# Kernel tuning notes

Measured on AMD Instinct MI355X. Metric: run time of the kernel, lower is better.

The kernel has to match this reference:

```python
import jax, jax.numpy as jnp
import numpy as np

B, DIM, H, W = 8, 128, 128, 128
QK, MLP, HEADS, NT, GS = 128, 256, 4, 8, 128


def _ln(x, w, b):
    m = jnp.mean(x, -1, keepdims=True)
    v = jnp.mean((x - m) ** 2, -1, keepdims=True)
    return (x - m) * jax.lax.rsqrt(v + 1e-5) * w + b


def _norml2(x):
    n = jnp.sqrt(jnp.sum(x * x, -1, keepdims=True))
    return x / jnp.maximum(n, 1e-12)


def setup_inputs() -> dict:
    key = jax.random.key(0)
    ks = jax.random.split(key, 12)
    s = 0.02
    f32 = jnp.float32
    return {
        'x': jax.random.normal(ks[0], (B, DIM, H, W), f32),
        'means': jax.random.normal(ks[1], (NT, DIM), f32),
        'ln1_w': jnp.ones((DIM,), f32), 'ln1_b': jnp.zeros((DIM,), f32),
        'wq': jax.random.normal(ks[2], (QK, DIM), f32) * s,
        'wk': jax.random.normal(ks[3], (QK, DIM), f32) * s,
        'wv': jax.random.normal(ks[4], (DIM, DIM), f32) * s,
        'wproj': jax.random.normal(ks[5], (DIM, DIM), f32) * s,
        'irca_wk': jax.random.normal(ks[6], (QK, DIM), f32) * s,
        'irca_wv': jax.random.normal(ks[7], (DIM, DIM), f32) * s,
        'conv1x1_w': jax.random.normal(ks[8], (DIM, DIM), f32) * s,
        'ln2_w': jnp.ones((DIM,), f32), 'ln2_b': jnp.zeros((DIM,), f32),
        'fc1_w': jax.random.normal(ks[9], (MLP, DIM), f32) * s,
        'fc1_b': jnp.zeros((MLP,), f32),
        'dw_w': jax.random.normal(ks[10], (MLP, 1, 5, 5), f32) * s,
        'dw_b': jnp.zeros((MLP,), f32),
        'fc2_w': jax.random.normal(ks[11], (DIM, MLP), f32) * s,
        'fc2_b': jnp.zeros((DIM,), f32),
    }


def reference(x, means, ln1_w, ln1_b, wq, wk, wv, wproj, irca_wk, irca_wv,
              conv1x1_w, ln2_w, ln2_b, fc1_w, fc1_b, dw_w, dw_b, fc2_w, fc2_b):
    Bx, C, Hh, Ww = x.shape
    N = Hh * Ww
    xt = x.reshape(Bx, C, N).transpose(0, 2, 1)          # b n c
    residual = xt
    xn = _ln(xt, ln1_w, ln1_b)
    m = jax.lax.stop_gradient(means)                      # eval: means buffer, detached
    # IRCA (eval path): global K/V from cluster means
    dq, dv = QK // HEADS, C // HEADS
    kg = (m @ irca_wk.T).reshape(NT, HEADS, dq).transpose(1, 0, 2)  # h nt dq
    vg = (m @ irca_wv.T).reshape(NT, HEADS, dv).transpose(1, 0, 2)  # h nt dv
    # cluster assignment -> token reordering (no grad)
    scores = jnp.einsum('bic,jc->bij', _norml2(xn), _norml2(m))
    buckets = jnp.argmax(scores, axis=-1)
    idx = jnp.argsort(buckets, axis=-1)                   # [B,N] permutation
    # IASA
    q = xn @ wq.T
    k = xn @ wk.T
    v = xn @ wv.T
    take = lambda t: jnp.take_along_axis(t, idx[:, :, None], axis=1)
    q, k, v = take(q), take(k), take(v)
    gs = min(N, GS)
    ng = (N + gs - 1) // gs
    pad_n = ng * gs - N
    qp = jnp.concatenate([q, jnp.flip(q[:, N - pad_n:N], axis=1)], axis=1)
    qp = qp.reshape(Bx, ng, gs, HEADS, dq).transpose(0, 1, 3, 2, 4)  # b g h gs dq

    def window(t, d):
        tp = jnp.concatenate([t, jnp.flip(t[:, N - pad_n - gs:N], axis=1)], axis=1)
        blk = tp.reshape(Bx, ng + 1, gs, HEADS, d)
        win = jnp.concatenate([blk[:, :-1], blk[:, 1:]], axis=2)     # b g 2gs h d
        return win.transpose(0, 1, 3, 2, 4)

    kp = window(k, dq)
    vp = window(v, dv)
    scale = 1.0 / np.sqrt(dq)
    a1 = jax.nn.softmax(jnp.einsum('bghqd,bghkd->bghqk', qp, kp) * scale, axis=-1)
    out1 = jnp.einsum('bghqk,bghkd->bghqd', a1, vp)
    a2 = jax.nn.softmax(jnp.einsum('bghqd,hkd->bghqk', qp, kg) * scale, axis=-1)
    out2 = jnp.einsum('bghqk,hkd->bghqd', a2, vg)
    out = (out1 + out2).transpose(0, 1, 3, 2, 4).reshape(Bx, ng * gs, C)[:, :N]
    inv = jnp.argsort(idx, axis=-1)                       # scatter-back = inverse perm
    out = jnp.take_along_axis(out, inv[:, :, None], axis=1)
    out = out @ wproj.T
    yimg = out.transpose(0, 2, 1).reshape(Bx, C, Hh, Ww)
    yimg = jnp.einsum('oc,bchw->bohw', conv1x1_w, yimg)
    x2 = residual + yimg.reshape(Bx, C, N).transpose(0, 2, 1)
    # ConvFFN with PreNorm
    xm = _ln(x2, ln2_w, ln2_b)
    h1 = jax.nn.gelu(xm @ fc1_w.T + fc1_b, approximate=False)
    himg = h1.transpose(0, 2, 1).reshape(Bx, MLP, Hh, Ww)
    dwc = jax.lax.conv_general_dilated(himg, dw_w, (1, 1), 'SAME',
                                       feature_group_count=MLP,
                                       dimension_numbers=('NCHW', 'OIHW', 'NCHW'))
    dwc = jax.nn.gelu(dwc + dw_b.reshape(1, MLP, 1, 1), approximate=False)
    h1 = h1 + dwc.reshape(Bx, MLP, N).transpose(0, 2, 1)
    x3 = x2 + (h1 @ fc2_w.T + fc2_b)
    return x3.transpose(0, 2, 1).reshape(Bx, C, Hh, Ww)
```

## Files before the change

kernel.cpp:

```cpp
#include <hip/hip_runtime.h>
#include <math.h>

typedef unsigned short u16;
typedef unsigned int u32;
typedef __attribute__((ext_vector_type(8))) short bf16x8;
typedef __attribute__((ext_vector_type(4))) float f32x4;

constexpr int BB   = 8;
constexpr int DIMC = 128;
constexpr int HH   = 128;
constexpr int WW   = 128;
constexpr int NTOK = HH * WW;
constexpr int QKD  = 128;
constexpr int MLPD = 256;
constexpr int NTm  = 8;
constexpr int GSZ  = 128;
constexpr int NGRP = NTOK / GSZ;
constexpr size_t BIG = 16777216;

__device__ __forceinline__ float gelu_f(float v) {
    return 0.5f * v * (1.0f + erff(v * 0.70710678118654752440f));
}
__device__ __forceinline__ float b2f(u16 u) {
    return __uint_as_float(((u32)u) << 16);
}
__device__ __forceinline__ u16 f2b(float f) {
    u32 x = __float_as_uint(f);
    return (u16)((x + 0x7fffu + ((x >> 16) & 1u)) >> 16);
}
__device__ __forceinline__ float ulo(u32 u) { return __uint_as_float(u << 16); }
__device__ __forceinline__ float uhi(u32 u) { return __uint_as_float(u & 0xffff0000u); }

__global__ __launch_bounds__(128) void k_prep(const float* __restrict__ means,
        const float* __restrict__ iwk, const float* __restrict__ iwv,
        float* __restrict__ mhat, u16* __restrict__ kgbb, u16* __restrict__ vgtb) {
    __shared__ float sm[DIMC];
    __shared__ float inv_s;
    int tt = blockIdx.x;
    int t = threadIdx.x;
    sm[t] = means[tt * DIMC + t];
    __syncthreads();
    if (t == 0) {
        float s = 0.f;
        for (int c = 0; c < DIMC; c++) s += sm[c] * sm[c];
        inv_s = 1.f / fmaxf(sqrtf(s), 1e-12f);
    }
    __syncthreads();
    mhat[tt * DIMC + t] = sm[t] * inv_s;
    float sk = 0.f, sv = 0.f;
    #pragma unroll 8
    for (int c = 0; c < DIMC; c++) {
        sk = fmaf(sm[c], iwk[t * DIMC + c], sk);
        sv = fmaf(sm[c], iwv[t * DIMC + c], sv);
    }
    kgbb[tt * DIMC + t] = f2b(sk);
    vgtb[(t >> 5) * 256 + (t & 31) * 8 + tt] = f2b(sv);
}

__global__ __launch_bounds__(256) void k_cvtall(const float* __restrict__ wq,
        const float* __restrict__ wk, const float* __restrict__ wv,
        const float* __restrict__ fc1, const float* __restrict__ fc2,
        u16* __restrict__ wqkv, u16* __restrict__ fc1b, u16* __restrict__ fc2b) {
    int i = blockIdx.x * 256 + threadIdx.x;
    if (i < 49152) {
        const float* s = (i < 16384) ? wq : (i < 32768 ? wk : wv);
        wqkv[i] = f2b(s[i & 16383]);
    } else if (i < 81920) {
        fc1b[i - 49152] = f2b(fc1[i - 49152]);
    } else if (i < 114688) {
        fc2b[i - 81920] = f2b(fc2[i - 81920]);
    }
}

__global__ __launch_bounds__(256) void k_fuse(const float* __restrict__ c1,
        const float* __restrict__ wp, u16* __restrict__ wf) {
    __shared__ float wpS[DIMC * DIMC];
    int t = threadIdx.x;
    for (int i = t; i < DIMC * DIMC; i += 256) wpS[i] = wp[i];
    __syncthreads();
    int o = blockIdx.x * 2 + (t >> 7);
    int c = t & 127;
    float s = 0.f;
    #pragma unroll 8
    for (int m = 0; m < DIMC; m++) s = fmaf(c1[o * DIMC + m], wpS[m * DIMC + c], s);
    wf[o * DIMC + c] = f2b(s);
}

__global__ __launch_bounds__(256) void k_ln1(const float* __restrict__ x,
        const float* __restrict__ lw, const float* __restrict__ lb,
        const float* __restrict__ mhat, u16* __restrict__ xn, int* __restrict__ bucket) {
    __shared__ float smh[NTm * DIMC];
    __shared__ float lwb[DIMC], lbb[DIMC];
    __shared__ float red[4][64][3];
    __shared__ float scr[4][64][9];
    const int chunk = blockIdx.x;
    const int b = chunk >> 8;
    const int n0 = (chunk & 255) << 6;
    const int t = threadIdx.x;
    const int cg = t >> 6, tok = t & 63;
    const int n = n0 + tok;
    const int cbase = cg * 32;
    for (int i = t; i < NTm * DIMC; i += 256) smh[i] = mhat[i];
    if (t < DIMC) { lwb[t] = lw[t]; lbb[t] = lb[t]; }

    const float* xb = x + (size_t)b * DIMC * NTOK + (size_t)cbase * NTOK + n;
    float xv[32];
    float sum = 0.f, sq = 0.f;
    #pragma unroll
    for (int c = 0; c < 32; c++) {
        float v = xb[(size_t)c * NTOK];
        xv[c] = v;
        sum += v; sq += v * v;
    }
    red[cg][tok][0] = sum;
    red[cg][tok][1] = sq;
    __syncthreads();
    float s0 = red[0][tok][0] + red[1][tok][0] + red[2][tok][0] + red[3][tok][0];
    float q0 = red[0][tok][1] + red[1][tok][1] + red[2][tok][1] + red[3][tok][1];
    float mean = s0 * (1.0f / DIMC);
    float var = q0 * (1.0f / DIMC) - mean * mean;
    float rstd = rsqrtf(var + 1e-5f);

    float sc[NTm];
    #pragma unroll
    for (int j = 0; j < NTm; j++) sc[j] = 0.f;
    u32 opk[16];
    #pragma unroll
    for (int c = 0; c < 32; c += 2) {
        float v0 = (xv[c]     - mean) * rstd * lwb[cbase + c]     + lbb[cbase + c];
        float v1 = (xv[c + 1] - mean) * rstd * lwb[cbase + c + 1] + lbb[cbase + c + 1];
        #pragma unroll
        for (int j = 0; j < NTm; j++) {
            sc[j] = fmaf(v0, smh[j * DIMC + cbase + c], sc[j]);
            sc[j] = fmaf(v1, smh[j * DIMC + cbase + c + 1], sc[j]);
        }
        opk[c >> 1] = (u32)f2b(v0) | ((u32)f2b(v1) << 16);
    }
    u16* xnr = xn + ((size_t)b * NTOK + n) * DIMC + cbase;
    *(uint4*)(xnr + 0)  = make_uint4(opk[0],  opk[1],  opk[2],  opk[3]);
    *(uint4*)(xnr + 8)  = make_uint4(opk[4],  opk[5],  opk[6],  opk[7]);
    *(uint4*)(xnr + 16) = make_uint4(opk[8],  opk[9],  opk[10], opk[11]);
    *(uint4*)(xnr + 24) = make_uint4(opk[12], opk[13], opk[14], opk[15]);

    #pragma unroll
    for (int j = 0; j < NTm; j++) scr[cg][tok][j] = sc[j];
    __syncthreads();
    if (cg == 0) {
        int best = 0; float bv = 0.f;
        #pragma unroll
        for (int j = 0; j < NTm; j++) {
            float v = ((scr[0][tok][j] + scr[1][tok][j]) +
                       (scr[2][tok][j] + scr[3][tok][j]));
            if (j == 0 || v > bv) { bv = v; best = (v > bv || j == 0) ? ((j == 0) ? 0 : j) : best; }
        }
        float v0 = ((scr[0][tok][0] + scr[1][tok][0]) + (scr[2][tok][0] + scr[3][tok][0]));
        best = 0; bv = v0;
        #pragma unroll
        for (int j = 1; j < NTm; j++) {
            float v = ((scr[0][tok][j] + scr[1][tok][j]) + (scr[2][tok][j] + scr[3][tok][j]));
            if (v > bv) { bv = v; best = j; }
        }
        bucket[b * NTOK + n] = best;
    }
}

__global__ __launch_bounds__(64) void k_count(const int* __restrict__ bucket, int* __restrict__ cnt) {
    int chunk = blockIdx.x;
    int bk = bucket[(chunk << 6) + threadIdx.x];
    #pragma unroll
    for (int j = 0; j < NTm; j++) {
        unsigned long long m = __ballot(bk == j);
        if (threadIdx.x == 0) cnt[chunk * NTm + j] = (int)__popcll(m);
    }
}

__global__ __launch_bounds__(64) void k_scan(const int* __restrict__ cnt, int* __restrict__ base) {
    __shared__ int sc[256 * NTm];
    __shared__ int bb[NTm], tot[NTm];
    int b = blockIdx.x, t = threadIdx.x;
    for (int i = t; i < 256 * NTm; i += 64) sc[i] = cnt[b * 256 * NTm + i];
    __syncthreads();
    if (t < NTm) {
        int run = 0;
        for (int c = 0; c < 256; c++) {
            int v = sc[c * NTm + t];
            sc[c * NTm + t] = run;
            run += v;
        }
        tot[t] = run;
    }
    __syncthreads();
    if (t == 0) {
        int a = 0;
        for (int j = 0; j < NTm; j++) { bb[j] = a; a += tot[j]; }
    }
    __syncthreads();
    for (int i = t; i < 256 * NTm; i += 64) base[b * 256 * NTm + i] = sc[i] + bb[i & 7];
}

__global__ __launch_bounds__(64) void k_place(const int* __restrict__ bucket,
        const int* __restrict__ base, int* __restrict__ gidx) {
    int chunk = blockIdx.x;
    int lane = threadIdx.x;
    int nf = (chunk << 6) + lane;
    int bk = bucket[nf];
    unsigned long long lower = (1ull << lane) - 1ull;
    int rank = 0;
    #pragma unroll
    for (int j = 0; j < NTm; j++) {
        unsigned long long m = __ballot(bk == j);
        if (bk == j) rank = (int)__popcll(m & lower);
    }
    int b = nf >> 14;
    int pos = base[chunk * NTm + bk] + rank;
    gidx[b * NTOK + pos] = nf & (NTOK - 1);
}

__global__ __launch_bounds__(256) void k_inv(const int* __restrict__ gidx, u16* __restrict__ iinv) {
    int i = blockIdx.x * 256 + threadIdx.x;
    int b = i >> 14;
    iinv[((size_t)b << 14) + gidx[i]] = (u16)(i & (NTOK - 1));
}

template<int KDIM, int NOUT, int GATHER, int AIMG, int BIASF, int GELUF, int RES, int STIMG, int CBF, int LN2F>
__global__ __launch_bounds__(256) void g_mfma(const u16* __restrict__ A, const u16* __restrict__ W,
        const float* __restrict__ bias, const void* __restrict__ resid,
        const int* __restrict__ gidx, void* __restrict__ Cout, float ascale,
        const float* __restrict__ lnw, const float* __restrict__ lnb, void* __restrict__ Cout2) {
    __shared__ u16 As[128 * 40];
    __shared__ u16 Ws[128 * 40];
    const int b = blockIdx.z;
    const int m0 = blockIdx.x * 128;
    const int n0 = blockIdx.y * 128;
    const int t = threadIdx.x;
    const int lane = t & 63;
    const int wave = t >> 6;
    const int wm = (wave & 1) * 64;
    const int wn = (wave >> 1) * 64;
    const int srow = t >> 2;
    const int sko = (t & 3) * 8;
    const u16* pA0 = nullptr; const u16* pA1 = nullptr;
    if (!AIMG) {
        int ra0 = m0 + srow, ra1 = m0 + 64 + srow;
        if (GATHER == 1) {
            ra0 = gidx[b * NTOK + ra0];
            ra1 = gidx[b * NTOK + ra1];
        } else if (GATHER == 2) {
            const u16* gi = (const u16*)gidx;
            ra0 = gi[b * NTOK + ra0];
            ra1 = gi[b * NTOK + ra1];
        }
        pA0 = A + ((size_t)b * NTOK + ra0) * KDIM + sko;
        pA1 = A + ((size_t)b * NTOK + ra1) * KDIM + sko;
    }
    const u16* pW0 = W + (size_t)(n0 + srow) * KDIM + sko;
    const u16* pW1 = W + (size_t)(n0 + 64 + srow) * KDIM + sko;

    f32x4 acc[4][4];
    #pragma unroll
    for (int i = 0; i < 4; i++)
        #pragma unroll
        for (int j = 0; j < 4; j++) acc[i][j] = (f32x4){0.f, 0.f, 0.f, 0.f};

    for (int k0 = 0; k0 < KDIM; k0 += 32) {
        uint4 a0, a1, w0, w1;
        u16 e[16];
        if (!AIMG) {
            a0 = *(const uint4*)(pA0 + k0);
            a1 = *(const uint4*)(pA1 + k0);
        } else {
            const int kk2 = t & 31;
            const int tg = t >> 5;
            const u16* src = A + ((size_t)b * KDIM + k0 + kk2) * NTOK + m0 + tg * 16;
            *(uint4*)&e[0] = *(const uint4*)src;
            *(uint4*)&e[8] = *(const uint4*)(src + 8);
        }
        w0 = *(const uint4*)(pW0 + k0);
        w1 = *(const uint4*)(pW1 + k0);
        __syncthreads();
        if (!AIMG) {
            *(uint4*)&As[srow * 40 + sko] = a0;
            *(uint4*)&As[(64 + srow) * 40 + sko] = a1;
        } else {
            const int kk2 = t & 31;
            const int tg = t >> 5;
            #pragma unroll
            for (int j = 0; j < 16; j++) As[(tg * 16 + j) * 40 + kk2] = e[j];
        }
        *(uint4*)&Ws[srow * 40 + sko] = w0;
        *(uint4*)&Ws[(64 + srow) * 40 + sko] = w1;
        __syncthreads();
        bf16x8 af[4], bfv[4];
        #pragma unroll
        for (int i = 0; i < 4; i++)
            af[i] = *(bf16x8*)&As[(wm + i * 16 + (lane & 15)) * 40 + (lane >> 4) * 8];
        #pragma unroll
        for (int j = 0; j < 4; j++)
            bfv[j] = *(bf16x8*)&Ws[(wn + j * 16 + (lane & 15)) * 40 + (lane >> 4) * 8];
        #pragma unroll
        for (int i = 0; i < 4; i++)
            #pragma unroll
            for (int j = 0; j < 4; j++)
                acc[i][j] = __builtin_amdgcn_mfma_f32_16x16x32_bf16(af[i], bfv[j], acc[i][j], 0, 0, 0);
    }

    const int c2 = lane & 15, gq2 = lane >> 4;
    int colj[4];
    #pragma unroll
    for (int j = 0; j < 4; j++) colj[j] = n0 + wn + j * 16 + c2;

    if (LN2F) {
        #pragma unroll
        for (int i = 0; i < 4; i++) {
            int rbase = m0 + wm + i * 16 + gq2 * 4;
            #pragma unroll
            for (int j = 0; j < 4; j++) {
                const float* rf = (const float*)resid;
                float4 rr = *(const float4*)&rf[((size_t)b * NOUT + colj[j]) * NTOK + rbase];
                acc[i][j][0] += rr.x; acc[i][j][1] += rr.y;
                acc[i][j][2] += rr.z; acc[i][j][3] += rr.w;
            }
        }
        __syncthreads();
        float* ps = (float*)&As[0];
        const int h = wn >> 6;
        float mean_[4][4], rstd_[4][4];
        #pragma unroll
        for (int i = 0; i < 4; i++)
            #pragma unroll
            for (int r = 0; r < 4; r++) {
                float s = 0.f, q = 0.f;
                #pragma unroll
                for (int j = 0; j < 4; j++) { float tv = acc[i][j][r]; s += tv; q += tv * tv; }
                s += __shfl_xor(s, 1, 64); q += __shfl_xor(q, 1, 64);
                s += __shfl_xor(s, 2, 64); q += __shfl_xor(q, 2, 64);
                s += __shfl_xor(s, 4, 64); q += __shfl_xor(q, 4, 64);
                s += __shfl_xor(s, 8, 64); q += __shfl_xor(q, 8, 64);
                if (c2 == 0) {
                    int rl = wm + i * 16 + gq2 * 4 + r;
                    ps[(h * 128 + rl) * 2 + 0] = s;
                    ps[(h * 128 + rl) * 2 + 1] = q;
                }
            }
        __syncthreads();
        #pragma unroll
        for (int i = 0; i < 4; i++)
            #pragma unroll
            for (int r = 0; r < 4; r++) {
                int rl = wm + i * 16 + gq2 * 4 + r;
                float s = ps[rl * 2 + 0] + ps[(128 + rl) * 2 + 0];
                float q = ps[rl * 2 + 1] + ps[(128 + rl) * 2 + 1];
                float mn = s * (1.0f / 128.0f);
                float vr = q * (1.0f / 128.0f) - mn * mn;
                mean_[i][r] = mn;
                rstd_[i][r] = rsqrtf(vr + 1e-5f);
            }
        float lwj[4], lbj[4];
        #pragma unroll
        for (int j = 0; j < 4; j++) { lwj[j] = lnw[colj[j]]; lbj[j] = lnb[colj[j]]; }
        u16* xo = (u16*)Cout;
        u16* mo = (u16*)Cout2;
        #pragma unroll
        for (int i = 0; i < 4; i++) {
            int rbase = m0 + wm + i * 16 + gq2 * 4;
            #pragma unroll
            for (int j = 0; j < 4; j++)
                #pragma unroll
                for (int r = 0; r < 4; r++) {
                    float tv = acc[i][j][r];
                    size_t off = ((size_t)b * NTOK + rbase + r) * NOUT + colj[j];
                    xo[off] = f2b(tv);
                    mo[off] = f2b((tv - mean_[i][r]) * rstd_[i][r] * lwj[j] + lbj[j]);
                }
        }
        return;
    }

    const float smul = (blockIdx.y == 0) ? ascale : 1.0f;
    float bj[4];
    #pragma unroll
    for (int j = 0; j < 4; j++) bj[j] = BIASF ? bias[colj[j]] : 0.f;
    #pragma unroll
    for (int i = 0; i < 4; i++) {
        int rbase = m0 + wm + i * 16 + gq2 * 4;
        #pragma unroll
        for (int j = 0; j < 4; j++) {
            f32x4 v = acc[i][j];
            v[0] *= smul; v[1] *= smul; v[2] *= smul; v[3] *= smul;
            if (BIASF) { v[0] += bj[j]; v[1] += bj[j]; v[2] += bj[j]; v[3] += bj[j]; }
            if (GELUF) { v[0] = gelu_f(v[0]); v[1] = gelu_f(v[1]); v[2] = gelu_f(v[2]); v[3] = gelu_f(v[3]); }
            if (RES == 1) {
                const float* rf = (const float*)resid;
                float4 rr = *(const float4*)&rf[((size_t)b * NOUT + colj[j]) * NTOK + rbase];
                v[0] += rr.x; v[1] += rr.y; v[2] += rr.z; v[3] += rr.w;
            } else if (RES == 3) {
                const u16* rb = (const u16*)resid;
                #pragma unroll
                for (int r = 0; r < 4; r++)
                    v[r] += b2f(rb[((size_t)b * NTOK + rbase + r) * NOUT + colj[j]]);
            }
            if (STIMG) {
                size_t off = ((size_t)b * NOUT + colj[j]) * NTOK + rbase;
                if (CBF) {
                    ushort4 o;
                    o.x = f2b(v[0]); o.y = f2b(v[1]); o.z = f2b(v[2]); o.w = f2b(v[3]);
                    *(ushort4*)((u16*)Cout + off) = o;
                } else {
                    *(float4*)((float*)Cout + off) = make_float4(v[0], v[1], v[2], v[3]);
                }
            } else {
                if (CBF) {
                    #pragma unroll
                    for (int r = 0; r < 4; r++)
                        ((u16*)Cout)[((size_t)b * NTOK + rbase + r) * NOUT + colj[j]] = f2b(v[r]);
                } else {
                    #pragma unroll
                    for (int r = 0; r < 4; r++)
                        ((float*)Cout)[((size_t)b * NTOK + rbase + r) * NOUT + colj[j]] = v[r];
                }
            }
        }
    }
}

__global__ __launch_bounds__(256, 3) void k_attn(const u16* __restrict__ qkv,
        const u16* __restrict__ kgbb, const u16* __restrict__ vgtb,
        u16* __restrict__ outp) {
    __shared__ u16 VT[2][32][264];
    __shared__ u16 Pb[4][64][40];
    const int g = blockIdx.x, hp = blockIdx.y, b = blockIdx.z;
    const int t = threadIdx.x;
    const int wave = t >> 6, lane = t & 63;
    const int c = lane & 15, gq = lane >> 4;
    const int lh = wave & 1, head = hp * 2 + lh, qh = wave >> 1;
    const size_t brow = (size_t)b * NTOK;

    {
        int key = t;
        int pos = (key < GSZ) ? g * GSZ + key
                : (g == NGRP - 1 ? NTOK - 1 - (key - GSZ) : g * GSZ + key);
        const u16* vp = qkv + (brow + pos) * 384 + 256 + hp * 64;
        #pragma unroll
        for (int i = 0; i < 8; i++) {
            uint4 v = *(const uint4*)(vp + i * 8);
            u16 e[8];
            *(uint4*)e = v;
            #pragma unroll
            for (int j = 0; j < 8; j++) {
                int d = i * 8 + j;
                VT[d >> 5][d & 31][key] = e[j];
            }
        }
        if (t < 64) {
            int l2 = t >> 5, dv = t & 31;
            uint4 v = *(const uint4*)(vgtb + ((size_t)(hp * 2 + l2) * 32 + dv) * 8);
            *(uint4*)&VT[l2][dv][256] = v;
        }
    }

    const int q0 = g * GSZ + qh * 64;
    bf16x8 qf[4];
    #pragma unroll
    for (int nq = 0; nq < 4; nq++)
        qf[nq] = *(const bf16x8*)(qkv + (brow + q0 + nq * 16 + c) * 384 + head * 32 + gq * 8);

    const u16* kbp = qkv + brow * 384 + 128 + head * 32 + gq * 8;
    bf16x8 kfa[8][2];
    #pragma unroll
    for (int s = 0; s < 8; s++)
        #pragma unroll
        for (int mk = 0; mk < 2; mk++) {
            int kl = s * 32 + mk * 16 + c;
            int pos = (kl < GSZ) ? g * GSZ + kl
                    : (g == NGRP - 1 ? NTOK - 1 - (kl - GSZ) : g * GSZ + kl);
            kfa[s][mk] = *(const bf16x8*)(kbp + (size_t)pos * 384);
        }
    bf16x8 kgf = *(const bf16x8*)(kgbb + (c & 7) * 128 + head * 32 + gq * 8);

    __syncthreads();

    f32x4 acc[4][2];
    #pragma unroll
    for (int i = 0; i < 4; i++)
        #pragma unroll
        for (int j = 0; j < 2; j++) acc[i][j] = (f32x4){0.f, 0.f, 0.f, 0.f};
    float lsum[4] = {0.f, 0.f, 0.f, 0.f};

    for (int s = 0; s < 8; s++) {
        #pragma unroll
        for (int mk = 0; mk < 2; mk++) {
            #pragma unroll
            for (int nq = 0; nq < 4; nq++) {
                f32x4 st = __builtin_amdgcn_mfma_f32_16x16x32_bf16(kfa[s][mk], qf[nq],
                        (f32x4){0.f, 0.f, 0.f, 0.f}, 0, 0, 0);
                float p0 = __expf(st[0]), p1 = __expf(st[1]);
                float p2 = __expf(st[2]), p3 = __expf(st[3]);
                lsum[nq] += (p0 + p1) + (p2 + p3);
                u32 r0, r1;
                asm("v_cvt_pk_bf16_f32 %0, %1, %2" : "=v"(r0) : "v"(p0), "v"(p1));
                asm("v_cvt_pk_bf16_f32 %0, %1, %2" : "=v"(r1) : "v"(p2), "v"(p3));
                *(uint2*)&Pb[wave][nq * 16 + c][mk * 16 + gq * 4] = make_uint2(r0, r1);
            }
        }
        __builtin_amdgcn_sched_barrier(0);
        bf16x8 pf[4], vf[2];
        #pragma unroll
        for (int mt = 0; mt < 4; mt++)
            pf[mt] = *(const bf16x8*)&Pb[wave][mt * 16 + c][gq * 8];
        #pragma unroll
        for (int nv = 0; nv < 2; nv++)
            vf[nv] = *(const bf16x8*)&VT[lh][nv * 16 + c][s * 32 + gq * 8];
        #pragma unroll
        for (int mt = 0; mt < 4; mt++)
            #pragma unroll
            for (int nv = 0; nv < 2; nv++)
                acc[mt][nv] = __builtin_amdgcn_mfma_f32_16x16x32_bf16(pf[mt], vf[nv], acc[mt][nv], 0, 0, 0);
    }

    #pragma unroll
    for (int nq = 0; nq < 4; nq++) {
        lsum[nq] += __shfl_xor(lsum[nq], 16, 64);
        lsum[nq] += __shfl_xor(lsum[nq], 32, 64);
    }

    {
        #pragma unroll
        for (int nq = 0; nq < 4; nq++) {
            f32x4 sg = __builtin_amdgcn_mfma_f32_16x16x32_bf16(kgf, qf[nq],
                    (f32x4){0.f, 0.f, 0.f, 0.f}, 0, 0, 0);
            float p0, p1, p2, p3;
            if (gq < 2) {
                p0 = __expf(sg[0]); p1 = __expf(sg[1]);
                p2 = __expf(sg[2]); p3 = __expf(sg[3]);
            } else { p0 = p1 = p2 = p3 = 0.f; }
            float lg = (p0 + p1) + (p2 + p3);
            lg += __shfl_xor(lg, 16, 64);
            lg += __shfl_xor(lg, 32, 64);
            float w = lsum[nq] / lg;
            p0 *= w; p1 *= w; p2 *= w; p3 *= w;
            u32 r0, r1;
            asm("v_cvt_pk_bf16_f32 %0, %1, %2" : "=v"(r0) : "v"(p0), "v"(p1));
            asm("v_cvt_pk_bf16_f32 %0, %1, %2" : "=v"(r1) : "v"(p2), "v"(p3));
            *(uint2*)&Pb[wave][nq * 16 + c][gq * 4] = make_uint2(r0, r1);
        }
        __builtin_amdgcn_sched_barrier(0);
        bf16x8 zf;
        #pragma unroll
        for (int z8 = 0; z8 < 8; z8++) zf[z8] = 0;
        bf16x8 pf[4], vf[2];
        #pragma unroll
        for (int mt = 0; mt < 4; mt++)
            pf[mt] = *(const bf16x8*)&Pb[wave][mt * 16 + c][gq * 8];
        #pragma unroll
        for (int nv = 0; nv < 2; nv++)
            vf[nv] = (gq == 0) ? *(const bf16x8*)&VT[lh][nv * 16 + c][256] : zf;
        #pragma unroll
        for (int mt = 0; mt < 4; mt++)
            #pragma unroll
            for (int nv = 0; nv < 2; nv++)
                acc[mt][nv] = __builtin_amdgcn_mfma_f32_16x16x32_bf16(pf[mt], vf[nv], acc[mt][nv], 0, 0, 0);
    }

    float* lf = (float*)&Pb[wave][0][0];
    if (gq == 0) {
        #pragma unroll
        for (int nq = 0; nq < 4; nq++) lf[nq * 16 + c] = lsum[nq];
    }
    __builtin_amdgcn_sched_barrier(0);
    u16 ov[4][2][4];
    #pragma unroll
    for (int mt = 0; mt < 4; mt++) {
        float il[4];
        #pragma unroll
        for (int r = 0; r < 4; r++)
            il[r] = 1.f / lf[mt * 16 + gq * 4 + r];
        #pragma unroll
        for (int nv = 0; nv < 2; nv++)
            #pragma unroll
            for (int r = 0; r < 4; r++)
                ov[mt][nv][r] = f2b(acc[mt][nv][r] * il[r]);
    }

    __syncthreads();
    u16* st = (u16*)&VT[0][0][0];
    #pragma unroll
    for (int mt = 0; mt < 4; mt++)
        #pragma unroll
        for (int nv = 0; nv < 2; nv++)
            #pragma unroll
            for (int r = 0; r < 4; r++)
                st[(qh * 64 + mt * 16 + gq * 4 + r) * 68 + lh * 32 + nv * 16 + c] = ov[mt][nv][r];
    __syncthreads();
    {
        const int rl0 = t >> 3;
        const int seg = t & 7;
        #pragma unroll
        for (int p = 0; p < 4; p++) {
            int rl = rl0 + p * 32;
            uint4 v4 = *(const uint4*)&st[rl * 68 + seg * 8];
            *(uint4*)&outp[(brow + g * GSZ + rl) * 128 + hp * 64 + seg * 8] = v4;
        }
    }
}

__global__ __launch_bounds__(256) void k_dw(const u16* __restrict__ himg,
        const float* __restrict__ dww, const float* __restrict__ dwb, u16* __restrict__ dsum) {
    const int mc = blockIdx.y, b = blockIdx.z;
    const int t = threadIdx.x;
    const int y = blockIdx.x * 32 + (t >> 4) * 2;
    const int xb = (t & 15) * 8;
    float wgt[25];
    #pragma unroll
    for (int i = 0; i < 25; i++) wgt[i] = dww[mc * 25 + i];
    const float bsv = dwb[mc];
    const u16* src = himg + ((size_t)b * MLPD + mc) * NTOK;
    u16* dst = dsum + ((size_t)b * MLPD + mc) * NTOK;

    float w[6][12];
    #pragma unroll
    for (int r = 0; r < 6; r++) {
        int ysrc = y - 2 + r;
        bool vy = (ysrc >= 0 && ysrc < HH);
        const u16* rp = src + ysrc * WW + xb;
        uint4 aq = vy ? *(const uint4*)(rp - 8) : make_uint4(0u, 0u, 0u, 0u);
        uint4 bq = vy ? *(const uint4*)(rp)     : make_uint4(0u, 0u, 0u, 0u);
        uint4 cq = vy ? *(const uint4*)(rp + 8) : make_uint4(0u, 0u, 0u, 0u);
        w[r][0]  = ulo(aq.w); w[r][1]  = uhi(aq.w);
        w[r][2]  = ulo(bq.x); w[r][3]  = uhi(bq.x);
        w[r][4]  = ulo(bq.y); w[r][5]  = uhi(bq.y);
        w[r][6]  = ulo(bq.z); w[r][7]  = uhi(bq.z);
        w[r][8]  = ulo(bq.w); w[r][9]  = uhi(bq.w);
        w[r][10] = ulo(cq.x); w[r][11] = uhi(cq.x);
        if (xb == 0)   { w[r][0]  = 0.f; w[r][1]  = 0.f; }
        if (xb == 120) { w[r][10] = 0.f; w[r][11] = 0.f; }
    }

    float acc0[8], acc1[8];
    #pragma unroll
    for (int px = 0; px < 8; px++) { acc0[px] = 0.f; acc1[px] = 0.f; }
    #pragma unroll
    for (int dy = 0; dy < 5; dy++)
        #pragma unroll
        for (int dx = 0; dx < 5; dx++) {
            float wv = wgt[dy * 5 + dx];
            #pragma unroll
            for (int px = 0; px < 8; px++) {
                acc0[px] = fmaf(wv, w[dy][px + dx], acc0[px]);
                acc1[px] = fmaf(wv, w[dy + 1][px + dx], acc1[px]);
            }
        }

    u32 o0[4], o1[4];
    #pragma unroll
    for (int px = 0; px < 8; px += 2) {
        u16 a0 = f2b(w[2][px + 2] + gelu_f(acc0[px] + bsv));
        u16 a1 = f2b(w[2][px + 3] + gelu_f(acc0[px + 1] + bsv));
        o0[px >> 1] = (u32)a0 | ((u32)a1 << 16);
        u16 b0 = f2b(w[3][px + 2] + gelu_f(acc1[px] + bsv));
        u16 b1 = f2b(w[3][px + 3] + gelu_f(acc1[px + 1] + bsv));
        o1[px >> 1] = (u32)b0 | ((u32)b1 << 16);
    }
    *(uint4*)(dst + y * WW + xb) = *(uint4*)o0;
    *(uint4*)(dst + (y + 1) * WW + xb) = *(uint4*)o1;
}

extern "C" void kernel_launch(void* const* d_in, const int* in_sizes, int n_in,
                              void* d_out, int out_size, void* d_ws, size_t ws_size,
                              hipStream_t stream) {
    const float* x       = (const float*)d_in[0];
    const float* means   = (const float*)d_in[1];
    const float* ln1_w   = (const float*)d_in[2];
    const float* ln1_b   = (const float*)d_in[3];
    const float* wq      = (const float*)d_in[4];
    const float* wk      = (const float*)d_in[5];
    const float* wv      = (const float*)d_in[6];
    const float* wproj   = (const float*)d_in[7];
    const float* irca_wk = (const float*)d_in[8];
    const float* irca_wv = (const float*)d_in[9];
    const float* conv1w  = (const float*)d_in[10];
    const float* ln2_w   = (const float*)d_in[11];
    const float* ln2_b   = (const float*)d_in[12];
    const float* fc1_w   = (const float*)d_in[13];
    const float* fc1_b   = (const float*)d_in[14];
    const float* dw_w    = (const float*)d_in[15];
    const float* dw_b    = (const float*)d_in[16];
    const float* fc2_w   = (const float*)d_in[17];
    const float* fc2_b   = (const float*)d_in[18];
    float* out = (float*)d_out;

    const size_t need = 202514432;
    if (ws_size < need) return;

    char* base = (char*)d_ws;
    float* mhat  = (float*)(base);
    u16*   kgbb  = (u16*)(base + 4096);
    u16*   vgtb  = (u16*)(base + 6144);
    int*   bucket = (int*)(base + 8192);
    u16*   wqkv  = (u16*)(base + 8192);
    u16*   wfub  = wqkv + 3 * 16384;
    u16*   fc1b  = wfub + 16384;
    u16*   fc2b  = fc1b + 32768;
    u16*   iinv  = (u16*)(base + 270336);
    int*   cnt   = (int*)(base + 532480);
    int*   cbase = (int*)(base + 598016);
    int*   gidx  = (int*)(base + 663552);
    u16*   Abase = (u16*)(base + 1187840);
    u16*   x2b   = (u16*)(base + 101851136);
    u16*   dsum  = (u16*)(base + 135405568);

    u16* qkv  = Abase;
    u16* himg = Abase;
    u16* xmb  = Abase + 2 * BIG;
    u16* xnb   = (u16*)d_out;
    u16* attnb = (u16*)d_out;

    k_prep<<<NTm, 128, 0, stream>>>(means, irca_wk, irca_wv, mhat, kgbb, vgtb);
    k_ln1<<<BB * NTOK / 64, 256, 0, stream>>>(x, ln1_w, ln1_b, mhat, xnb, bucket);
    k_count<<<BB * NTOK / 64, 64, 0, stream>>>(bucket, cnt);
    k_scan<<<BB, 64, 0, stream>>>(cnt, cbase);
    k_place<<<BB * NTOK / 64, 64, 0, stream>>>(bucket, cbase, gidx);
    k_inv<<<BB * NTOK / 256, 256, 0, stream>>>(gidx, iinv);

    k_cvtall<<<448, 256, 0, stream>>>(wq, wk, wv, fc1_w, fc2_w, wqkv, fc1b, fc2b);
    k_fuse<<<64, 256, 0, stream>>>(conv1w, wproj, wfub);

    const float qsc = 0.17677669529663687f;
    g_mfma<128, 384, 1, 0, 0, 0, 0, 0, 1, 0><<<dim3(128, 3, BB), 256, 0, stream>>>(
        xnb, wqkv, nullptr, nullptr, gidx, qkv, qsc, nullptr, nullptr, nullptr);

    k_attn<<<dim3(NGRP, 2, BB), 256, 0, stream>>>(qkv, kgbb, vgtb, attnb);

    g_mfma<128, 128, 2, 0, 0, 0, 1, 0, 1, 1><<<dim3(128, 1, BB), 256, 0, stream>>>(
        attnb, wfub, nullptr, x, (const int*)iinv, x2b, 1.0f, ln2_w, ln2_b, xmb);

    g_mfma<128, 256, 0, 0, 1, 1, 0, 1, 1, 0><<<dim3(128, 2, BB), 256, 0, stream>>>(
        xmb, fc1b, fc1_b, nullptr, nullptr, himg, 1.0f, nullptr, nullptr, nullptr);
    k_dw<<<dim3(4, MLPD, BB), 256, 0, stream>>>(himg, dw_w, dw_b, dsum);
    g_mfma<256, 128, 0, 1, 1, 0, 3, 1, 0, 0><<<dim3(128, 1, BB), 256, 0, stream>>>(
        dsum, fc2b, fc2_b, x2b, nullptr, out, 1.0f, nullptr, nullptr, nullptr);

    (void)in_sizes; (void)n_in; (void)out_size;
}
```

Baseline: 321.9 us.

## Split QKV projection, store V channel-major for attention, use exp2 softmax

The fused QKV GEMM is split into a Q/K GEMM with 256-wide rows and a separate V GEMM that writes a transposed, channel-major V image. The attention kernel can then fill its transposed V tile in shared memory with vector row copies instead of scattering scalar elements. The last group's mirrored tail keys are handled by reading a reversed chunk and flipping it. The Q scale is folded with log2(e) so the softmax uses exp2f instead of __expf. A dead duplicate argmax loop in LN1 is also removed. This adds an extra GEMM launch and a second read of the normalized input.

```diff
diff --git a/kernel.cpp b/kernel.cpp
--- a/kernel.cpp
+++ b/kernel.cpp
@@ -146,15 +146,8 @@
     for (int j = 0; j < NTm; j++) scr[cg][tok][j] = sc[j];
     __syncthreads();
     if (cg == 0) {
-        int best = 0; float bv = 0.f;
-        #pragma unroll
-        for (int j = 0; j < NTm; j++) {
-            float v = ((scr[0][tok][j] + scr[1][tok][j]) +
-                       (scr[2][tok][j] + scr[3][tok][j]));
-            if (j == 0 || v > bv) { bv = v; best = (v > bv || j == 0) ? ((j == 0) ? 0 : j) : best; }
-        }
         float v0 = ((scr[0][tok][0] + scr[1][tok][0]) + (scr[2][tok][0] + scr[3][tok][0]));
-        best = 0; bv = v0;
+        int best = 0; float bv = v0;
         #pragma unroll
         for (int j = 1; j < NTm; j++) {
             float v = ((scr[0][tok][j] + scr[1][tok][j]) + (scr[2][tok][j] + scr[3][tok][j]));
@@ -423,7 +416,8 @@
     }
 }
 
-__global__ __launch_bounds__(256, 3) void k_attn(const u16* __restrict__ qkv,
+__global__ __launch_bounds__(256, 3) void k_attn(const u16* __restrict__ qk,
+        const u16* __restrict__ vimg,
         const u16* __restrict__ kgbb, const u16* __restrict__ vgtb,
         u16* __restrict__ outp) {
     __shared__ u16 VT[2][32][264];
@@ -434,27 +428,34 @@
     const int c = lane & 15, gq = lane >> 4;
     const int lh = wave & 1, head = hp * 2 + lh, qh = wave >> 1;
     const size_t brow = (size_t)b * NTOK;
+    const bool lastg = (g == NGRP - 1);
 
     {
-        int key = t;
-        int pos = (key < GSZ) ? g * GSZ + key
-                : (g == NGRP - 1 ? NTOK - 1 - (key - GSZ) : g * GSZ + key);
-        const u16* vp = qkv + (brow + pos) * 384 + 256 + hp * 64;
-        #pragma unroll
-        for (int i = 0; i < 8; i++) {
-            uint4 v = *(const uint4*)(vp + i * 8);
-            u16 e[8];
-            *(uint4*)e = v;
-            #pragma unroll
-            for (int j = 0; j < 8; j++) {
-                int d = i * 8 + j;
-                VT[d >> 5][d & 31][key] = e[j];
+        const int dv = t >> 2;
+        const int kc = t & 3;
+        const u16* vrow = vimg + ((size_t)(b * 128 + hp * 64 + dv)) * NTOK;
+        u16* vtrow = (u16*)&VT[0][0][0] + dv * 264;
+        #pragma unroll
+        for (int p = 0; p < 8; p++) {
+            int chunk = p * 4 + kc;
+            int k0 = chunk * 8;
+            uint4 v;
+            if (!lastg || k0 < GSZ) {
+                v = *(const uint4*)(vrow + g * GSZ + k0);
+            } else {
+                uint4 r = *(const uint4*)(vrow + NTOK + 120 - k0);
+                u16 e[8], o[8];
+                *(uint4*)e = r;
+                #pragma unroll
+                for (int j = 0; j < 8; j++) o[j] = e[7 - j];
+                v = *(uint4*)o;
             }
+            *(uint4*)(vtrow + k0) = v;
         }
         if (t < 64) {
-            int l2 = t >> 5, dv = t & 31;
-            uint4 v = *(const uint4*)(vgtb + ((size_t)(hp * 2 + l2) * 32 + dv) * 8);
-            *(uint4*)&VT[l2][dv][256] = v;
+            int l2 = t >> 5, dvg = t & 31;
+            uint4 v = *(const uint4*)(vgtb + ((size_t)(hp * 2 + l2) * 32 + dvg) * 8);
+            *(uint4*)&VT[l2][dvg][256] = v;
         }
     }
 
@@ -462,18 +463,17 @@
     bf16x8 qf[4];
     #pragma unroll
     for (int nq = 0; nq < 4; nq++)
-        qf[nq] = *(const bf16x8*)(qkv + (brow + q0 + nq * 16 + c) * 384 + head * 32 + gq * 8);
-
-    const u16* kbp = qkv + brow * 384 + 128 + head * 32 + gq * 8;
+        qf[nq] = *(const bf16x8*)(qk + (brow + q0 + nq * 16 + c) * 256 + head * 32 + gq * 8);
+
+    const u16* kbp = qk + brow * 256 + 128 + head * 32 + gq * 8;
     bf16x8 kfa[8][2];
     #pragma unroll
     for (int s = 0; s < 8; s++)
         #pragma unroll
         for (int mk = 0; mk < 2; mk++) {
             int kl = s * 32 + mk * 16 + c;
-            int pos = (kl < GSZ) ? g * GSZ + kl
-                    : (g == NGRP - 1 ? NTOK - 1 - (kl - GSZ) : g * GSZ + kl);
-            kfa[s][mk] = *(const bf16x8*)(kbp + (size_t)pos * 384);
+            int pos = (!lastg || kl < GSZ) ? g * GSZ + kl : NTOK - 1 - (kl - GSZ);
+            kfa[s][mk] = *(const bf16x8*)(kbp + (size_t)pos * 256);
         }
     bf16x8 kgf = *(const bf16x8*)(kgbb + (c & 7) * 128 + head * 32 + gq * 8);
 
@@ -493,8 +493,8 @@
             for (int nq = 0; nq < 4; nq++) {
                 f32x4 st = __builtin_amdgcn_mfma_f32_16x16x32_bf16(kfa[s][mk], qf[nq],
                         (f32x4){0.f, 0.f, 0.f, 0.f}, 0, 0, 0);
-                float p0 = __expf(st[0]), p1 = __expf(st[1]);
-                float p2 = __expf(st[2]), p3 = __expf(st[3]);
+                float p0 = exp2f(st[0]), p1 = exp2f(st[1]);
+                float p2 = exp2f(st[2]), p3 = exp2f(st[3]);
                 lsum[nq] += (p0 + p1) + (p2 + p3);
                 u32 r0, r1;
                 asm("v_cvt_pk_bf16_f32 %0, %1, %2" : "=v"(r0) : "v"(p0), "v"(p1));
@@ -530,8 +530,8 @@
                     (f32x4){0.f, 0.f, 0.f, 0.f}, 0, 0, 0);
             float p0, p1, p2, p3;
             if (gq < 2) {
-                p0 = __expf(sg[0]); p1 = __expf(sg[1]);
-                p2 = __expf(sg[2]); p3 = __expf(sg[3]);
+                p0 = exp2f(sg[0]); p1 = exp2f(sg[1]);
+                p2 = exp2f(sg[2]); p3 = exp2f(sg[3]);
             } else { p0 = p1 = p2 = p3 = 0.f; }
             float lg = (p0 + p1) + (p2 + p3);
             lg += __shfl_xor(lg, 16, 64);
@@ -708,7 +708,8 @@
     u16*   x2b   = (u16*)(base + 101851136);
     u16*   dsum  = (u16*)(base + 135405568);
 
-    u16* qkv  = Abase;
+    u16* qkb  = Abase;
+    u16* vimg = Abase + 2 * BIG;
     u16* himg = Abase;
     u16* xmb  = Abase + 2 * BIG;
     u16* xnb   = (u16*)d_out;
@@ -724,11 +725,13 @@
     k_cvtall<<<448, 256, 0, stream>>>(wq, wk, wv, fc1_w, fc2_w, wqkv, fc1b, fc2b);
     k_fuse<<<64, 256, 0, stream>>>(conv1w, wproj, wfub);
 
-    const float qsc = 0.17677669529663687f;
-    g_mfma<128, 384, 1, 0, 0, 0, 0, 0, 1, 0><<<dim3(128, 3, BB), 256, 0, stream>>>(
-        xnb, wqkv, nullptr, nullptr, gidx, qkv, qsc, nullptr, nullptr, nullptr);
-
-    k_attn<<<dim3(NGRP, 2, BB), 256, 0, stream>>>(qkv, kgbb, vgtb, attnb);
+    const float qsc2 = 0.25503489924160945f;
+    g_mfma<128, 256, 1, 0, 0, 0, 0, 0, 1, 0><<<dim3(128, 2, BB), 256, 0, stream>>>(
+        xnb, wqkv, nullptr, nullptr, gidx, qkb, qsc2, nullptr, nullptr, nullptr);
+    g_mfma<128, 128, 1, 0, 0, 0, 0, 1, 1, 0><<<dim3(128, 1, BB), 256, 0, stream>>>(
+        xnb, wqkv + 2 * 16384, nullptr, nullptr, gidx, vimg, 1.0f, nullptr, nullptr, nullptr);
+
+    k_attn<<<dim3(NGRP, 2, BB), 256, 0, stream>>>(qkb, vimg, kgbb, vgtb, attnb);
 
     g_mfma<128, 128, 2, 0, 0, 0, 1, 0, 1, 1><<<dim3(128, 1, BB), 256, 0, stream>>>(
         attnb, wfub, nullptr, x, (const int*)iinv, x2b, 1.0f, ln2_w, ln2_b, xmb);
```

Result: slower. 341.8 us (+6.2%).
